# Kernel tuning notes

Hardware: AMD Instinct MI355X
Metric: run time of the kernel (lower is better)

The kernel has to match this reference:

```python
import jax, jax.numpy as jnp
import numpy as np

B, L, D, H = 1, 1024, 768, 12
h = D // H  # 64
EPS = 1e-5
ALPHA = 0.01  # leaky relu slope


def setup_inputs() -> dict:
    key = jax.random.key(0)
    ks = jax.random.split(key, 10)
    s = 0.02
    f32 = jnp.float32
    return {
        "x": jax.random.normal(ks[0], (B, L, D), f32),
        "filters": jax.random.normal(ks[1], (L, h), f32) * s,  # spectral filters [L, h]
        "wq_w": jax.random.normal(ks[2], (D, D), f32) * s,
        "wq_b": jnp.zeros((D,), f32),
        "wk_w": jax.random.normal(ks[3], (D, D), f32) * s,
        "wk_b": jnp.zeros((D,), f32),
        "wv_w": jax.random.normal(ks[4], (D, D), f32) * s,
        "wv_b": jnp.zeros((D,), f32),
        "wo_w": jax.random.normal(ks[5], (D, D), f32) * s,
        "wo_b": jnp.zeros((D,), f32),
        "wg_w": jax.random.normal(ks[6], (h * h, 1), f32) * s,
        "wg_b": jnp.zeros((1,), f32),
        "qk_scale": jnp.ones((1, H, 1), f32) + jax.random.normal(ks[7], (1, H, 1), f32) * 0.02,
        "kv_scale": jnp.ones((1, H, 1, 1, 1), f32) + jax.random.normal(ks[8], (1, H, 1, 1, 1), f32) * 0.02,
    }


def _causal_fft_conv(f, u):
    """Per-head-channel causal FFT convolution. f: [L,h], u: [B,H,L,h] -> [B,H,L,h]."""
    n = 2 * L  # >= L + L - 1 for linear (full) convolution
    Ff = jnp.fft.rfft(f, n=n, axis=0)            # [n//2+1, h]
    Uf = jnp.fft.rfft(u, n=n, axis=2)            # [B,H,n//2+1,h]
    y = jnp.fft.irfft(Uf * Ff[None, None], n=n, axis=2)
    return y[:, :, :L, :]


def _l2norm(t):
    # matches F.normalize(dim=-1): x / max(||x||, 1e-12)
    nrm = jnp.sqrt(jnp.sum(t * t, axis=-1, keepdims=True))
    return t / jnp.maximum(nrm, 1e-12)


def _combine(a, b):
    """Associative combine: (m, s, n, Z, g) running-max / exp-sum / exp-weighted-v / outer-product / gate-sum."""
    m_x, s_x, n_x, Z_x, g_x = a
    m_y, s_y, n_y, Z_y, g_y = b
    m = jnp.maximum(m_x, m_y)
    ex = jnp.exp(m_x - m)
    ey = jnp.exp(m_y - m)
    return (m,
            s_x * ex + s_y * ey,
            n_x * ex[..., None] + n_y * ey[..., None],
            Z_x + Z_y,
            g_x + g_y)


def reference(x, filters, wq_w, wq_b, wk_w, wk_b, wv_w, wv_b, wo_w, wo_b,
              wg_w, wg_b, qk_scale, kv_scale):
    # split heads: [B,H,L,h]
    bhld = x.reshape(B, L, H, h).transpose(0, 2, 1, 3)
    # spectral filtering (tensordot_conv): per-channel causal conv with filters
    xt = _causal_fft_conv(filters, bhld)                       # [B,H,L,h]
    xt = xt.transpose(0, 2, 1, 3).reshape(B, L, D)             # [B,L,D]

    q = (xt @ wq_w + wq_b).reshape(B, L, H, h).transpose(0, 2, 1, 3)
    k = (xt @ wk_w + wk_b).reshape(B, L, H, h).transpose(0, 2, 1, 3)
    v = (xt @ wv_w + wv_b).reshape(B, L, H, h).transpose(0, 2, 1, 3)
    q, k, v = _l2norm(q), _l2norm(k), _l2norm(v)

    sim = jnp.einsum('bhld,bhld->bhl', q, k) * qk_scale         # [B,H,L]
    # Z[b,h,s,p,n] = v[b,h,s,p] * k[b,h,s,n]
    Z = jnp.einsum('bhsn,bhsp->bhspn', k, v) * kv_scale         # [B,H,L,h,h]

    gate_logits = Z.reshape(B, H, L, h * h) @ wg_w + wg_b       # [B,H,L,1]
    gl = jnp.where(gate_logits > 0, gate_logits, ALPHA * gate_logits)
    gates = (gl * gl + EPS)[..., 0]                             # [B,H,L]
    gated_Z = Z * gates[..., None, None]

    leaves = (sim, jnp.ones_like(sim), v, gated_Z, gates)
    m_s, s_s, n_s, Z_s, g_s = jax.lax.associative_scan(_combine, leaves, axis=2)

    linear_attn = n_s / (s_s[..., None] + EPS)                  # [B,H,L,h]
    softmax_w = jnp.exp(sim - m_s) / (s_s + EPS)                # [B,H,L]
    Hm = Z_s / (g_s[..., None, None] + EPS)                     # [B,H,L,h,h]
    ctx = jnp.einsum('bhtp,bhtpn->bhtn', q, Hm)                 # [B,H,L,h]
    qla = linear_attn
    lerp = ctx + (qla - ctx) * softmax_w[..., None]

    y = lerp.transpose(0, 2, 1, 3).reshape(B, L, D)
    return y @ wo_w + wo_b
```

## Files before the change

### kernel.cpp

```cpp
#include <hip/hip_runtime.h>
#include <hip/hip_bf16.h>

constexpr int LS = 1024;
constexpr int DM = 768;
constexpr int NH = 12;
constexpr int HD = 64;
constexpr float EPSF = 1e-5f;
constexpr float ALPHAF = 0.01f;

constexpr int SG = 16;
constexpr int NTL = LS / SG;
constexpr int WSZ = DM * DM;
constexpr int NPAR = 8;

typedef unsigned short u16;
typedef __attribute__((ext_vector_type(8))) short bf16x8;
typedef __attribute__((ext_vector_type(8))) unsigned short u16x8;
typedef __attribute__((ext_vector_type(4))) float f32x4;

__device__ __forceinline__ u16 f2b(float f) {
  unsigned u = __float_as_uint(f);
  u += 0x7FFFu + ((u >> 16) & 1u);
  return (u16)(u >> 16);
}

__device__ __forceinline__ void gld16(const u16* g, void* l) {
  __builtin_amdgcn_global_load_lds(
      (const __attribute__((address_space(1))) void*)g,
      (__attribute__((address_space(3))) void*)l, 16, 0, 0);
}

__global__ __launch_bounds__(256) void conv_txw_kernel(
    const float* __restrict__ x, const float* __restrict__ f,
    const float* __restrict__ wq, const float* __restrict__ wk,
    const float* __restrict__ wv, const float* __restrict__ wo,
    u16* __restrict__ wT, float* __restrict__ pbase) {
  extern __shared__ char smem[];
  const int b = blockIdx.x;
  const int tid = threadIdx.x;

  if (b >= 1536) {
    const int b2 = b - 1536;
    const int kb = (b2 % 12) * 64, nb = ((b2 / 12) % 12) * 64, z = b2 / 144;
    const float* src = (z == 0) ? wq : (z == 1) ? wk : (z == 2) ? wv : wo;
    u16* dst = wT + (size_t)z * WSZ;
    float (*T)[65] = (float(*)[65])smem;
#pragma unroll
    for (int rep = 0; rep < 4; ++rep) {
      const int r = rep * 16 + (tid >> 4);
      const int c4 = (tid & 15) * 4;
      const float4 v4 = *(const float4*)(src + (size_t)(kb + r) * DM + nb + c4);
      T[r][c4] = v4.x; T[r][c4 + 1] = v4.y; T[r][c4 + 2] = v4.z; T[r][c4 + 3] = v4.w;
    }
    __syncthreads();
#pragma unroll
    for (int rep = 0; rep < 4; ++rep) {
      const int n = rep * 16 + (tid >> 4);
      const int k4 = (tid & 15) * 4;
      ushort4 o;
      o.x = f2b(T[k4 + 0][n]); o.y = f2b(T[k4 + 1][n]);
      o.z = f2b(T[k4 + 2][n]); o.w = f2b(T[k4 + 3][n]);
      *(ushort4*)(dst + (size_t)(nb + n) * DM + kb + k4) = o;
    }
    return;
  }

  const int i    = b & 15;
  const int head = (b >> 4) % 12;
  const int par  = b / 192;
  const int c    = tid & 63;
  const int sg   = tid >> 6;
  const int tbase = i * 64;
  const int l0w   = tbase + sg * 16;
  float* __restrict__ xt_p = pbase + (size_t)par * LS * DM;

  float4 (*Xs2)[64] = (float4(*)[64])smem;

  {
    const float4 z4 = make_float4(0.f, 0.f, 0.f, 0.f);
#pragma unroll
    for (int k = 0; k < 3; ++k) {
      const int lin = k * 256 + tid;
      const int g   = lin >> 6;
      const int cc  = lin & 63;
      const int grp = (g < 4) ? g : (16 + g);
      Xs2[grp][cc] = z4;
    }
  }

  float acc[16];
#pragma unroll
  for (int t = 0; t < 16; ++t) acc[t] = 0.f;

  const float* xg   = x + head * HD + c;
  const float* fcol = f + c;

  for (int j = par; j <= i; j += NPAR) {
    const int sbase = j * 64;
    const int b0 = (j < i) ? (tbase - sbase - 64) : 0;
#pragma unroll
    for (int k = 0; k < 4; ++k) {
      const int m  = sg + 4 * k;
      const int ss = 4 * m;
      float4 v4;
      v4.x = xg[(sbase + ss + 0) * DM];
      v4.y = xg[(sbase + ss + 1) * DM];
      v4.z = xg[(sbase + ss + 2) * DM];
      v4.w = xg[(sbase + ss + 3) * DM];
      Xs2[4 + m][c] = v4;
    }
    __syncthreads();

    const int dstart = (j < i) ? (b0 + sg * 16) : 0;
    const int nsteps = (j < i) ? 5 : (sg + 1);
    for (int k = 0; k < nsteps; ++k) {
      const int d0    = dstart + 16 * k;
      const int rbase = l0w - d0 - sbase;
      float fr[16];
#pragma unroll
      for (int m = 0; m < 16; ++m) fr[m] = fcol[(d0 + m) * HD];
      float xw[32];
      const int xgb = rbase >> 2;
#pragma unroll
      for (int m = 0; m < 8; ++m) {
        const float4 v4 = Xs2[xgb + m][c];
        xw[4 * m + 0] = v4.x; xw[4 * m + 1] = v4.y;
        xw[4 * m + 2] = v4.z; xw[4 * m + 3] = v4.w;
      }
#pragma unroll
      for (int li = 0; li < 16; ++li)
#pragma unroll
        for (int dd = 0; dd < 16; ++dd)
          acc[li] = fmaf(fr[dd], xw[li - dd + 16], acc[li]);
    }
    __syncthreads();
  }

#pragma unroll
  for (int li = 0; li < 16; ++li)
    xt_p[(size_t)(l0w + li) * DM + head * HD + c] = acc[li];
}

__global__ __launch_bounds__(256) void pack_xt(const float* __restrict__ pbase,
                                               u16* __restrict__ xtb) {
  const size_t NT = (size_t)LS * DM;
  const size_t i = ((size_t)blockIdx.x * 256 + threadIdx.x) * 8;
  u16x8 o;
#pragma unroll
  for (int h = 0; h < 2; ++h) {
    float4 s = make_float4(0.f, 0.f, 0.f, 0.f);
#pragma unroll
    for (int p = 0; p < NPAR; ++p) {
      const float4 v4 = *(const float4*)(pbase + p * NT + i + h * 4);
      s.x += v4.x; s.y += v4.y; s.z += v4.z; s.w += v4.w;
    }
    o[h * 4 + 0] = f2b(s.x); o[h * 4 + 1] = f2b(s.y);
    o[h * 4 + 2] = f2b(s.z); o[h * 4 + 3] = f2b(s.w);
  }
  *(u16x8*)(xtb + i) = o;
}

__global__ __launch_bounds__(256) void qkv_mfma(const u16* __restrict__ xtb,
                                                const u16* __restrict__ wT,
                                                const float* __restrict__ bq,
                                                const float* __restrict__ bk,
                                                const float* __restrict__ bv,
                                                float* __restrict__ qo,
                                                float* __restrict__ ko,
                                                float* __restrict__ vo) {
  const int b = blockIdx.x;
  const int xcd = b & 7, j = b >> 3;
  const int unit = xcd * 9 + (j >> 3), sub = j & 7;
  const int z = unit / 24, rem = unit % 24;
  const int ct = rem >> 1, rt = (rem & 1) * 8 + sub;

  __shared__ u16 As[64 * 64];
  __shared__ u16 Bs[64 * 64];

  const int tid = threadIdx.x, w = tid >> 6, l = tid & 63;
  const int wr = w >> 1, wc = w & 1;

  const int srow1 = tid >> 3, sc16 = tid & 7;
  const int c16L1 = sc16 ^ (srow1 & 7);
  const int srow2 = srow1 + 32;
  const int c16L2 = sc16 ^ (srow2 & 7);

  const u16* wz = wT + (size_t)z * WSZ;
  const u16* Ag1 = xtb + (size_t)(rt * 64 + srow1) * DM + c16L1 * 8;
  const u16* Ag2 = xtb + (size_t)(rt * 64 + srow2) * DM + c16L2 * 8;
  const u16* Bg1 = wz + (size_t)(ct * 64 + srow1) * DM + c16L1 * 8;
  const u16* Bg2 = wz + (size_t)(ct * 64 + srow2) * DM + c16L2 * 8;

  char* lA = (char*)As + w * 1024;
  char* lB = (char*)Bs + w * 1024;

  f32x4 acc[2][2] = {};
  for (int kb = 0; kb < DM; kb += 64) {
    gld16(Ag1 + kb, lA);
    gld16(Ag2 + kb, lA + 4096);
    gld16(Bg1 + kb, lB);
    gld16(Bg2 + kb, lB + 4096);
    __syncthreads();
#pragma unroll
    for (int kk = 0; kk < 2; ++kk) {
      bf16x8 a[2], bb[2];
#pragma unroll
      for (int ar = 0; ar < 2; ++ar) {
        const int row = wr * 32 + ar * 16 + (l & 15);
        const int c16 = ((kk << 2) + (l >> 4)) ^ (row & 7);
        a[ar] = *(const bf16x8*)((char*)As + row * 128 + c16 * 16);
      }
#pragma unroll
      for (int bc = 0; bc < 2; ++bc) {
        const int col = wc * 32 + bc * 16 + (l & 15);
        const int c16 = ((kk << 2) + (l >> 4)) ^ (col & 7);
        bb[bc] = *(const bf16x8*)((char*)Bs + col * 128 + c16 * 16);
      }
#pragma unroll
      for (int ar = 0; ar < 2; ++ar)
#pragma unroll
        for (int bc = 0; bc < 2; ++bc)
          acc[ar][bc] = __builtin_amdgcn_mfma_f32_16x16x32_bf16(
              a[ar], bb[bc], acc[ar][bc], 0, 0, 0);
    }
    __syncthreads();
  }

  const float* bias = (z == 0) ? bq : (z == 1) ? bk : bv;
  float* out = (z == 0) ? qo : (z == 1) ? ko : vo;
  const int rbase = rt * 64 + wr * 32 + ((l >> 4) << 2);
  const int cb = wc * 32 + (l & 15);
#pragma unroll
  for (int ar = 0; ar < 2; ++ar)
#pragma unroll
    for (int bc = 0; bc < 2; ++bc) {
      const int col = cb + bc * 16;
      const float bbv = bias[ct * 64 + col];
#pragma unroll
      for (int r = 0; r < 4; ++r)
        out[((size_t)ct * LS + rbase + ar * 16 + r) * HD + col] =
            acc[ar][bc][r] + bbv;
    }
}

__global__ __launch_bounds__(256) void out_mfma(const u16* __restrict__ lerpb,
                                                const u16* __restrict__ woT,
                                                const float* __restrict__ bias,
                                                float* __restrict__ out) {
  const int b = blockIdx.x;
  const int xcd = b & 7, j = b >> 3;
  const int unit = xcd * 3 + (j >> 3), sub = j & 7;
  const int ct = unit >> 1, rt = (unit & 1) * 8 + sub;

  __shared__ u16 As[64 * 64];
  __shared__ u16 Bs[64 * 64];

  const int tid = threadIdx.x, w = tid >> 6, l = tid & 63;
  const int wr = w >> 1, wc = w & 1;

  const int srow1 = tid >> 3, sc16 = tid & 7;
  const int c16L1 = sc16 ^ (srow1 & 7);
  const int srow2 = srow1 + 32;
  const int c16L2 = sc16 ^ (srow2 & 7);

  const u16* Ag1 = lerpb + (size_t)(rt * 64 + srow1) * DM + c16L1 * 8;
  const u16* Ag2 = lerpb + (size_t)(rt * 64 + srow2) * DM + c16L2 * 8;
  const u16* Bg1 = woT + (size_t)(ct * 64 + srow1) * DM + c16L1 * 8;
  const u16* Bg2 = woT + (size_t)(ct * 64 + srow2) * DM + c16L2 * 8;

  char* lA = (char*)As + w * 1024;
  char* lB = (char*)Bs + w * 1024;

  f32x4 acc[2][2] = {};
  for (int kb = 0; kb < DM; kb += 64) {
    gld16(Ag1 + kb, lA);
    gld16(Ag2 + kb, lA + 4096);
    gld16(Bg1 + kb, lB);
    gld16(Bg2 + kb, lB + 4096);
    __syncthreads();
#pragma unroll
    for (int kk = 0; kk < 2; ++kk) {
      bf16x8 a[2], bb[2];
#pragma unroll
      for (int ar = 0; ar < 2; ++ar) {
        const int row = wr * 32 + ar * 16 + (l & 15);
        const int c16 = ((kk << 2) + (l >> 4)) ^ (row & 7);
        a[ar] = *(const bf16x8*)((char*)As + row * 128 + c16 * 16);
      }
#pragma unroll
      for (int bc = 0; bc < 2; ++bc) {
        const int col = wc * 32 + bc * 16 + (l & 15);
        const int c16 = ((kk << 2) + (l >> 4)) ^ (col & 7);
        bb[bc] = *(const bf16x8*)((char*)Bs + col * 128 + c16 * 16);
      }
#pragma unroll
      for (int ar = 0; ar < 2; ++ar)
#pragma unroll
        for (int bc = 0; bc < 2; ++bc)
          acc[ar][bc] = __builtin_amdgcn_mfma_f32_16x16x32_bf16(
              a[ar], bb[bc], acc[ar][bc], 0, 0, 0);
    }
    __syncthreads();
  }

  const int rbase = rt * 64 + wr * 32 + ((l >> 4) << 2);
  const int cb = wc * 32 + (l & 15);
#pragma unroll
  for (int ar = 0; ar < 2; ++ar)
#pragma unroll
    for (int bc = 0; bc < 2; ++bc) {
      const int col = ct * 64 + cb + bc * 16;
      const float bbv = bias[col];
#pragma unroll
      for (int r = 0; r < 4; ++r)
        out[(size_t)(rbase + ar * 16 + r) * DM + col] = acc[ar][bc][r] + bbv;
    }
}

__global__ void norm_sim_gate(float* __restrict__ q, float* __restrict__ k, float* __restrict__ v,
                              const float* __restrict__ wg, const float* __restrict__ wgb,
                              const float* __restrict__ qk_scale, const float* __restrict__ kv_scale,
                              float* __restrict__ sim, float* __restrict__ gates) {
  const int w = threadIdx.x >> 6, lane = threadIdx.x & 63;
  const int l = blockIdx.x * 4 + w;
  const int head = blockIdx.y;
  const size_t idx = ((size_t)head * LS + l) * HD + lane;
  float qv = q[idx], kv = k[idx], vv = v[idx];

  auto red = [](float x) {
#pragma unroll
    for (int o = 32; o; o >>= 1) x += __shfl_xor(x, o);
    return x;
  };
  const float qn = fmaxf(sqrtf(red(qv * qv)), 1e-12f);
  const float kn = fmaxf(sqrtf(red(kv * kv)), 1e-12f);
  const float vn = fmaxf(sqrtf(red(vv * vv)), 1e-12f);
  qv /= qn; kv /= kn; vv /= vn;
  q[idx] = qv; k[idx] = kv; v[idx] = vv;

  const float s = red(qv * kv) * qk_scale[head];

  __shared__ float vs[4][64];
  vs[w][lane] = vv;
  __syncthreads();
  float t = 0.f;
#pragma unroll 8
  for (int p = 0; p < 64; ++p) t = fmaf(vs[w][p], wg[p * 64 + lane], t);
  float gl = red(t * kv) * kv_scale[head] + wgb[0];
  gl = gl > 0.f ? gl : ALPHAF * gl;
  const float g = gl * gl + EPSF;
  if (lane == 0) {
    sim[head * LS + l] = s;
    gates[head * LS + l] = g;
  }
}

__global__ void scan_kernel(const float* __restrict__ sim, const float* __restrict__ gates,
                            float* __restrict__ m_s, float* __restrict__ Sraw,
                            float* __restrict__ g_s) {
  const int head = blockIdx.x, t = threadIdx.x;
  __shared__ float bm[1024], bs[1024], bg[1024];
  const float sv = sim[head * LS + t];
  float m = sv, S = expf(sv), g = gates[head * LS + t];
  bm[t] = m; bs[t] = S; bg[t] = g;
  __syncthreads();
  for (int off = 1; off < 1024; off <<= 1) {
    float om = -1e30f, os = 0.f, og = 0.f;
    if (t >= off) { om = bm[t - off]; os = bs[t - off]; og = bg[t - off]; }
    __syncthreads();
    m = fmaxf(m, om); S += os; g += og;
    bm[t] = m; bs[t] = S; bg[t] = g;
    __syncthreads();
  }
  m_s[head * LS + t] = m;
  Sraw[head * LS + t] = S;
  g_s[head * LS + t] = g;
}

__global__ __launch_bounds__(256) void state_kernel(const float* __restrict__ k,
                                                    const float* __restrict__ v,
                                                    const float* __restrict__ sim,
                                                    const float* __restrict__ gates,
                                                    float* __restrict__ states,
                                                    float* __restrict__ nes) {
  const int j = blockIdx.x, head = blockIdx.y;
  const int s0 = j * SG;
  const int tid = threadIdx.x;
  __shared__ alignas(16) float Vs[SG][68];
  __shared__ alignas(16) float Kg[SG][68];
  __shared__ float Es[SG];

  const int r = tid >> 4, c = (tid & 15) * 4;
  const float* kh = k + ((size_t)head * LS + s0) * HD;
  const float* vh = v + ((size_t)head * LS + s0) * HD;
  const float g = gates[head * LS + s0 + r];
  *(float4*)&Vs[r][c] = *(const float4*)(vh + r * HD + c);
  float4 k4 = *(const float4*)(kh + r * HD + c);
  k4.x *= g; k4.y *= g; k4.z *= g; k4.w *= g;
  *(float4*)&Kg[r][c] = k4;
  if (tid < SG) Es[tid] = expf(sim[head * LS + s0 + tid]);
  __syncthreads();

  const int p0 = (tid >> 4) * 4, n0 = (tid & 15) * 4;
  float acc[4][4] = {};
  for (int s = 0; s < SG; ++s) {
    const float4 ra = *(const float4*)&Vs[s][p0];
    const float4 rb = *(const float4*)&Kg[s][n0];
    const float av[4] = {ra.x, ra.y, ra.z, ra.w};
    const float bv[4] = {rb.x, rb.y, rb.z, rb.w};
#pragma unroll
    for (int i = 0; i < 4; ++i)
#pragma unroll
      for (int jj = 0; jj < 4; ++jj)
        acc[i][jj] = fmaf(av[i], bv[jj], acc[i][jj]);
  }
  float* Sout = states + (size_t)(head * NTL + j) * 4096;
#pragma unroll
  for (int i = 0; i < 4; ++i)
    *(float4*)&Sout[(p0 + i) * 64 + n0] =
        make_float4(acc[i][0], acc[i][1], acc[i][2], acc[i][3]);

  if (tid < HD) {
    float ne = 0.f;
    for (int s = 0; s < SG; ++s) ne = fmaf(Es[s], Vs[s][tid], ne);
    nes[(size_t)(head * NTL + j) * HD + tid] = ne;
  }
}

__global__ __launch_bounds__(256) void prefix_kernel(float* __restrict__ states,
                                                     float* __restrict__ nes) {
  const int head = blockIdx.x, chunk = blockIdx.y;
  const int tid = threadIdx.x;
  const int off = chunk * 1024 + tid * 4;
  float4 acc = make_float4(0.f, 0.f, 0.f, 0.f);
  float* base = states + (size_t)head * NTL * 4096 + off;
#pragma unroll 4
  for (int j = 0; j < NTL; ++j) {
    float4* p = (float4*)(base + (size_t)j * 4096);
    const float4 sv = *p;
    *p = acc;
    acc.x += sv.x; acc.y += sv.y; acc.z += sv.z; acc.w += sv.w;
  }
  if (chunk == 0 && tid < HD) {
    float a = 0.f;
    float* nb = nes + (size_t)head * NTL * HD + tid;
#pragma unroll 4
    for (int j = 0; j < NTL; ++j) {
      float* p = nb + (size_t)j * HD;
      const float t = *p;
      *p = a;
      a += t;
    }
  }
}

__global__ __launch_bounds__(256) void apply_kernel(const float* __restrict__ q,
                                                    const float* __restrict__ k,
                                                    const float* __restrict__ v,
                                                    const float* __restrict__ sim,
                                                    const float* __restrict__ gates,
                                                    const float* __restrict__ m_s,
                                                    const float* __restrict__ Sraw,
                                                    const float* __restrict__ g_s,
                                                    const float* __restrict__ states,
                                                    const float* __restrict__ nes,
                                                    const float* __restrict__ kv_scale,
                                                    u16* __restrict__ lerpb) {
  const int bt = blockIdx.x, head = blockIdx.y;
  const int t0 = bt * SG;
  const int tid = threadIdx.x;
  __shared__ alignas(16) float Ps[64][68];
  __shared__ alignas(16) float Qs[SG][68];
  __shared__ alignas(16) float Vs[SG][68];
  __shared__ alignas(16) float Ks[SG][68];
  __shared__ alignas(16) float NEp[64];
  __shared__ float Ag[SG][SG + 1];
  __shared__ float Es[SG], Gs[SG];

  const float* Pg = states + (size_t)(head * NTL + bt) * 4096;
#pragma unroll
  for (int rep = 0; rep < 4; ++rep) {
    const int lin = rep * 1024 + tid * 4;
    *(float4*)&Ps[lin >> 6][lin & 63] = *(const float4*)(Pg + lin);
  }
  {
    const int r = tid >> 4, c = (tid & 15) * 4;
    const size_t rowbase = ((size_t)head * LS + t0 + r) * HD;
    *(float4*)&Qs[r][c] = *(const float4*)(q + rowbase + c);
    *(float4*)&Ks[r][c] = *(const float4*)(k + rowbase + c);
    *(float4*)&Vs[r][c] = *(const float4*)(v + rowbase + c);
  }
  if (tid < SG) {
    Es[tid] = expf(sim[head * LS + t0 + tid]);
    Gs[tid] = gates[head * LS + t0 + tid];
  }
  if (tid < HD) NEp[tid] = nes[(size_t)(head * NTL + bt) * HD + tid];
  __syncthreads();

  {
    const int t = tid >> 4, s = tid & 15;
    float a = 0.f;
    if (s <= t) {
#pragma unroll
      for (int p = 0; p < 64; p += 4) {
        const float4 q4 = *(const float4*)&Qs[t][p];
        const float4 v4 = *(const float4*)&Vs[s][p];
        a = fmaf(q4.x, v4.x, a); a = fmaf(q4.y, v4.y, a);
        a = fmaf(q4.z, v4.z, a); a = fmaf(q4.w, v4.w, a);
      }
      a *= Gs[s];
    }
    Ag[t][s] = a;
  }
  __syncthreads();

  const int r = tid >> 4, c0 = (tid & 15) * 4;
  float4 O = make_float4(0.f, 0.f, 0.f, 0.f);
#pragma unroll 8
  for (int p = 0; p < 64; ++p) {
    const float qv = Qs[r][p];
    const float4 p4 = *(const float4*)&Ps[p][c0];
    O.x = fmaf(qv, p4.x, O.x); O.y = fmaf(qv, p4.y, O.y);
    O.z = fmaf(qv, p4.z, O.z); O.w = fmaf(qv, p4.w, O.w);
  }
  float4 Nn = *(const float4*)&NEp[c0];
  for (int s = 0; s <= r; ++s) {
    const float ag = Ag[r][s];
    const float es = Es[s];
    const float4 k4 = *(const float4*)&Ks[s][c0];
    const float4 v4 = *(const float4*)&Vs[s][c0];
    O.x = fmaf(ag, k4.x, O.x); O.y = fmaf(ag, k4.y, O.y);
    O.z = fmaf(ag, k4.z, O.z); O.w = fmaf(ag, k4.w, O.w);
    Nn.x = fmaf(es, v4.x, Nn.x); Nn.y = fmaf(es, v4.y, Nn.y);
    Nn.z = fmaf(es, v4.z, Nn.z); Nn.w = fmaf(es, v4.w, Nn.w);
  }

  const int t = t0 + r;
  const float m  = m_s[head * LS + t];
  const float em = expf(-m);
  const float ss = Sraw[head * LS + t] * em;
  const float inv = 1.f / (ss + EPSF);
  const float sw  = expf(sim[head * LS + t] - m) * inv;
  const float gi  = kv_scale[head] / (g_s[head * LS + t] + EPSF);
  const float ei  = em * inv;
  float rx, ry, rz, rw;
  { const float cx = O.x * gi, la = Nn.x * ei; rx = cx + (la - cx) * sw; }
  { const float cx = O.y * gi, la = Nn.y * ei; ry = cx + (la - cx) * sw; }
  { const float cx = O.z * gi, la = Nn.z * ei; rz = cx + (la - cx) * sw; }
  { const float cx = O.w * gi, la = Nn.w * ei; rw = cx + (la - cx) * sw; }
  ushort4 ob;
  ob.x = f2b(rx); ob.y = f2b(ry); ob.z = f2b(rz); ob.w = f2b(rw);
  *(ushort4*)&lerpb[(size_t)t * DM + head * HD + c0] = ob;
}

extern "C" void kernel_launch(void* const* d_in, const int* in_sizes, int n_in,
                              void* d_out, int out_size, void* d_ws, size_t ws_size,
                              hipStream_t stream) {
  (void)in_sizes; (void)n_in; (void)out_size; (void)ws_size;
  const float* x        = (const float*)d_in[0];
  const float* filters  = (const float*)d_in[1];
  const float* wq_w     = (const float*)d_in[2];
  const float* wq_b     = (const float*)d_in[3];
  const float* wk_w     = (const float*)d_in[4];
  const float* wk_b     = (const float*)d_in[5];
  const float* wv_w     = (const float*)d_in[6];
  const float* wv_b     = (const float*)d_in[7];
  const float* wo_w     = (const float*)d_in[8];
  const float* wo_b     = (const float*)d_in[9];
  const float* wg_w     = (const float*)d_in[10];
  const float* wg_b     = (const float*)d_in[11];
  const float* qk_scale = (const float*)d_in[12];
  const float* kv_scale = (const float*)d_in[13];

  float* ws = (float*)d_ws;
  const size_t NT = (size_t)LS * DM;
  float* q     = ws;
  float* k     = ws + NT;
  float* v     = ws + 2 * NT;
  float* sim   = ws + 3 * NT;
  float* gates = sim + NH * LS;
  float* m_s   = gates + NH * LS;
  float* Sraw  = m_s + NH * LS;
  float* g_s   = Sraw + NH * LS;
  float* states = g_s + NH * LS;
  float* nes    = states + (size_t)NH * NTL * 4096;
  u16*   xtb    = (u16*)(nes + (size_t)NH * NTL * HD);
  u16*   wT     = xtb + NT;
  u16*   lerpb  = wT + 4 * (size_t)WSZ;
  float* pbase  = (float*)(lerpb + NT);

  conv_txw_kernel<<<dim3(2112), 256, 28672, stream>>>(
      x, filters, wq_w, wk_w, wv_w, wo_w, wT, pbase);
  pack_xt<<<dim3(NT / 2048), 256, 0, stream>>>(pbase, xtb);
  qkv_mfma<<<dim3(576), 256, 0, stream>>>(xtb, wT, wq_b, wk_b, wv_b, q, k, v);
  norm_sim_gate<<<dim3(LS / 4, NH), 256, 0, stream>>>(
      q, k, v, wg_w, wg_b, qk_scale, kv_scale, sim, gates);
  scan_kernel<<<dim3(NH), 1024, 0, stream>>>(sim, gates, m_s, Sraw, g_s);
  state_kernel<<<dim3(NTL, NH), 256, 0, stream>>>(k, v, sim, gates, states, nes);
  prefix_kernel<<<dim3(NH, 4), 256, 0, stream>>>(states, nes);
  apply_kernel<<<dim3(NTL, NH), 256, 0, stream>>>(
      q, k, v, sim, gates, m_s, Sraw, g_s, states, nes, kv_scale, lerpb);
  out_mfma<<<dim3(192), 256, 0, stream>>>(
      lerpb, wT + 3 * (size_t)WSZ, wo_b, (float*)d_out);
}
```

Baseline: 102.5 us.

## Fuse norm/gate into state kernel, fuse scan with prefix, store partials as bf16

Merges the per-row normalize/sim/gate computation into the chunk state kernel, which removes one launch and one global round trip of sim and gates. Merges the scan and prefix kernels into a single 1024-thread kernel whose scan uses warp shuffles with a cross-wave pass instead of a shared-memory Hillis-Steele loop. The conv partial sums are now stored as bf16 instead of fp32, halving pack traffic but adding rounding error before summation. The fused prefix runs on only 12 blocks instead of 48, which reduces parallelism for the state prefix sum.

Result: slower. 107.6 us (+5.0%).

```diff
diff --git a/kernel.cpp b/kernel.cpp
--- a/kernel.cpp
+++ b/kernel.cpp
@@ -23,6 +23,9 @@
   u += 0x7FFFu + ((u >> 16) & 1u);
   return (u16)(u >> 16);
 }
+__device__ __forceinline__ float b2f(u16 b) {
+  return __uint_as_float((unsigned)b << 16);
+}
 
 __device__ __forceinline__ void gld16(const u16* g, void* l) {
   __builtin_amdgcn_global_load_lds(
@@ -34,7 +37,7 @@
     const float* __restrict__ x, const float* __restrict__ f,
     const float* __restrict__ wq, const float* __restrict__ wk,
     const float* __restrict__ wv, const float* __restrict__ wo,
-    u16* __restrict__ wT, float* __restrict__ pbase) {
+    u16* __restrict__ wT, u16* __restrict__ pbase) {
   extern __shared__ char smem[];
   const int b = blockIdx.x;
   const int tid = threadIdx.x;
@@ -72,7 +75,7 @@
   const int sg   = tid >> 6;
   const int tbase = i * 64;
   const int l0w   = tbase + sg * 16;
-  float* __restrict__ xt_p = pbase + (size_t)par * LS * DM;
+  u16* __restrict__ xt_p = pbase + (size_t)par * LS * DM;
 
   float4 (*Xs2)[64] = (float4(*)[64])smem;
 
@@ -138,25 +141,23 @@
 
 #pragma unroll
   for (int li = 0; li < 16; ++li)
-    xt_p[(size_t)(l0w + li) * DM + head * HD + c] = acc[li];
-}
-
-__global__ __launch_bounds__(256) void pack_xt(const float* __restrict__ pbase,
+    xt_p[(size_t)(l0w + li) * DM + head * HD + c] = f2b(acc[li]);
+}
+
+__global__ __launch_bounds__(256) void pack_xt(const u16* __restrict__ pbase,
                                                u16* __restrict__ xtb) {
   const size_t NT = (size_t)LS * DM;
   const size_t i = ((size_t)blockIdx.x * 256 + threadIdx.x) * 8;
+  float s[8] = {};
+#pragma unroll
+  for (int p = 0; p < NPAR; ++p) {
+    const u16x8 v8 = *(const u16x8*)(pbase + p * NT + i);
+#pragma unroll
+    for (int e = 0; e < 8; ++e) s[e] += b2f(v8[e]);
+  }
   u16x8 o;
 #pragma unroll
-  for (int h = 0; h < 2; ++h) {
-    float4 s = make_float4(0.f, 0.f, 0.f, 0.f);
-#pragma unroll
-    for (int p = 0; p < NPAR; ++p) {
-      const float4 v4 = *(const float4*)(pbase + p * NT + i + h * 4);
-      s.x += v4.x; s.y += v4.y; s.z += v4.z; s.w += v4.w;
-    }
-    o[h * 4 + 0] = f2b(s.x); o[h * 4 + 1] = f2b(s.y);
-    o[h * 4 + 2] = f2b(s.z); o[h * 4 + 3] = f2b(s.w);
-  }
+  for (int e = 0; e < 8; ++e) o[e] = f2b(s[e]);
   *(u16x8*)(xtb + i) = o;
 }
 
@@ -317,88 +318,52 @@
     }
 }
 
-__global__ void norm_sim_gate(float* __restrict__ q, float* __restrict__ k, float* __restrict__ v,
-                              const float* __restrict__ wg, const float* __restrict__ wgb,
-                              const float* __restrict__ qk_scale, const float* __restrict__ kv_scale,
-                              float* __restrict__ sim, float* __restrict__ gates) {
-  const int w = threadIdx.x >> 6, lane = threadIdx.x & 63;
-  const int l = blockIdx.x * 4 + w;
-  const int head = blockIdx.y;
-  const size_t idx = ((size_t)head * LS + l) * HD + lane;
-  float qv = q[idx], kv = k[idx], vv = v[idx];
+__global__ __launch_bounds__(256) void nsg_state_kernel(
+    float* __restrict__ q, float* __restrict__ k, float* __restrict__ v,
+    const float* __restrict__ wg, const float* __restrict__ wgb,
+    const float* __restrict__ qk_scale, const float* __restrict__ kv_scale,
+    float* __restrict__ sim, float* __restrict__ gates,
+    float* __restrict__ states, float* __restrict__ nes) {
+  const int j = blockIdx.x, head = blockIdx.y;
+  const int s0 = j * SG;
+  const int tid = threadIdx.x;
+  const int wid = tid >> 6, lane = tid & 63;
+  __shared__ alignas(16) float Vs[SG][68];
+  __shared__ alignas(16) float Kg[SG][68];
+  __shared__ float Es[SG];
 
   auto red = [](float x) {
 #pragma unroll
     for (int o = 32; o; o >>= 1) x += __shfl_xor(x, o);
     return x;
   };
-  const float qn = fmaxf(sqrtf(red(qv * qv)), 1e-12f);
-  const float kn = fmaxf(sqrtf(red(kv * kv)), 1e-12f);
-  const float vn = fmaxf(sqrtf(red(vv * vv)), 1e-12f);
-  qv /= qn; kv /= kn; vv /= vn;
-  q[idx] = qv; k[idx] = kv; v[idx] = vv;
-
-  const float s = red(qv * kv) * qk_scale[head];
-
-  __shared__ float vs[4][64];
-  vs[w][lane] = vv;
-  __syncthreads();
-  float t = 0.f;
+
+  const float qks = qk_scale[head], kvs = kv_scale[head], wb = wgb[0];
+#pragma unroll
+  for (int it = 0; it < 4; ++it) {
+    const int rr = wid * 4 + it;
+    const size_t idx = ((size_t)head * LS + s0 + rr) * HD + lane;
+    float qv = q[idx], kv = k[idx], vv = v[idx];
+    const float qn = fmaxf(sqrtf(red(qv * qv)), 1e-12f);
+    const float kn = fmaxf(sqrtf(red(kv * kv)), 1e-12f);
+    const float vn = fmaxf(sqrtf(red(vv * vv)), 1e-12f);
+    qv /= qn; kv /= kn; vv /= vn;
+    q[idx] = qv; k[idx] = kv; v[idx] = vv;
+    const float s = red(qv * kv) * qks;
+    Vs[rr][lane] = vv;
+    float t = 0.f;
 #pragma unroll 8
-  for (int p = 0; p < 64; ++p) t = fmaf(vs[w][p], wg[p * 64 + lane], t);
-  float gl = red(t * kv) * kv_scale[head] + wgb[0];
-  gl = gl > 0.f ? gl : ALPHAF * gl;
-  const float g = gl * gl + EPSF;
-  if (lane == 0) {
-    sim[head * LS + l] = s;
-    gates[head * LS + l] = g;
-  }
-}
-
-__global__ void scan_kernel(const float* __restrict__ sim, const float* __restrict__ gates,
-                            float* __restrict__ m_s, float* __restrict__ Sraw,
-                            float* __restrict__ g_s) {
-  const int head = blockIdx.x, t = threadIdx.x;
-  __shared__ float bm[1024], bs[1024], bg[1024];
-  const float sv = sim[head * LS + t];
-  float m = sv, S = expf(sv), g = gates[head * LS + t];
-  bm[t] = m; bs[t] = S; bg[t] = g;
-  __syncthreads();
-  for (int off = 1; off < 1024; off <<= 1) {
-    float om = -1e30f, os = 0.f, og = 0.f;
-    if (t >= off) { om = bm[t - off]; os = bs[t - off]; og = bg[t - off]; }
-    __syncthreads();
-    m = fmaxf(m, om); S += os; g += og;
-    bm[t] = m; bs[t] = S; bg[t] = g;
-    __syncthreads();
-  }
-  m_s[head * LS + t] = m;
-  Sraw[head * LS + t] = S;
-  g_s[head * LS + t] = g;
-}
-
-__global__ __launch_bounds__(256) void state_kernel(const float* __restrict__ k,
-                                                    const float* __restrict__ v,
-                                                    const float* __restrict__ sim,
-                                                    const float* __restrict__ gates,
-                                                    float* __restrict__ states,
-                                                    float* __restrict__ nes) {
-  const int j = blockIdx.x, head = blockIdx.y;
-  const int s0 = j * SG;
-  const int tid = threadIdx.x;
-  __shared__ alignas(16) float Vs[SG][68];
-  __shared__ alignas(16) float Kg[SG][68];
-  __shared__ float Es[SG];
-
-  const int r = tid >> 4, c = (tid & 15) * 4;
-  const float* kh = k + ((size_t)head * LS + s0) * HD;
-  const float* vh = v + ((size_t)head * LS + s0) * HD;
-  const float g = gates[head * LS + s0 + r];
-  *(float4*)&Vs[r][c] = *(const float4*)(vh + r * HD + c);
-  float4 k4 = *(const float4*)(kh + r * HD + c);
-  k4.x *= g; k4.y *= g; k4.z *= g; k4.w *= g;
-  *(float4*)&Kg[r][c] = k4;
-  if (tid < SG) Es[tid] = expf(sim[head * LS + s0 + tid]);
+    for (int p = 0; p < 64; ++p) t = fmaf(Vs[rr][p], wg[p * 64 + lane], t);
+    float gl = red(t * kv) * kvs + wb;
+    gl = gl > 0.f ? gl : ALPHAF * gl;
+    const float g = gl * gl + EPSF;
+    Kg[rr][lane] = kv * g;
+    if (lane == 0) {
+      sim[head * LS + s0 + rr] = s;
+      gates[head * LS + s0 + rr] = g;
+      Es[rr] = expf(s);
+    }
+  }
   __syncthreads();
 
   const int p0 = (tid >> 4) * 4, n0 = (tid & 15) * 4;
@@ -422,31 +387,55 @@
 
   if (tid < HD) {
     float ne = 0.f;
+#pragma unroll
     for (int s = 0; s < SG; ++s) ne = fmaf(Es[s], Vs[s][tid], ne);
     nes[(size_t)(head * NTL + j) * HD + tid] = ne;
   }
 }
 
-__global__ __launch_bounds__(256) void prefix_kernel(float* __restrict__ states,
-                                                     float* __restrict__ nes) {
-  const int head = blockIdx.x, chunk = blockIdx.y;
-  const int tid = threadIdx.x;
-  const int off = chunk * 1024 + tid * 4;
-  float4 acc = make_float4(0.f, 0.f, 0.f, 0.f);
-  float* base = states + (size_t)head * NTL * 4096 + off;
+__global__ __launch_bounds__(1024) void scan_prefix_kernel(
+    const float* __restrict__ sim, const float* __restrict__ gates,
+    float* __restrict__ m_s, float* __restrict__ Sraw, float* __restrict__ g_s,
+    float* __restrict__ states, float* __restrict__ nes) {
+  const int head = blockIdx.x;
+  const int tid = threadIdx.x, lane = tid & 63, wid = tid >> 6;
+  __shared__ float wm[16], wS[16], wg2[16];
+
+  const float sv = sim[head * LS + tid];
+  float m = sv, S = expf(sv), g = gates[head * LS + tid];
+#pragma unroll
+  for (int off = 1; off < 64; off <<= 1) {
+    const float pm = __shfl_up(m, off);
+    const float pS = __shfl_up(S, off);
+    const float pg = __shfl_up(g, off);
+    if (lane >= off) { m = fmaxf(m, pm); S += pS; g += pg; }
+  }
+  if (lane == 63) { wm[wid] = m; wS[wid] = S; wg2[wid] = g; }
+  __syncthreads();
+  for (int w2 = 0; w2 < wid; ++w2) {
+    m = fmaxf(m, wm[w2]); S += wS[w2]; g += wg2[w2];
+  }
+  m_s[head * LS + tid] = m;
+  Sraw[head * LS + tid] = S;
+  g_s[head * LS + tid] = g;
+
+  {
+    float4 acc = make_float4(0.f, 0.f, 0.f, 0.f);
+    float* base = states + (size_t)head * NTL * 4096 + tid * 4;
 #pragma unroll 4
-  for (int j = 0; j < NTL; ++j) {
-    float4* p = (float4*)(base + (size_t)j * 4096);
-    const float4 sv = *p;
-    *p = acc;
-    acc.x += sv.x; acc.y += sv.y; acc.z += sv.z; acc.w += sv.w;
-  }
-  if (chunk == 0 && tid < HD) {
+    for (int jj = 0; jj < NTL; ++jj) {
+      float4* p = (float4*)(base + (size_t)jj * 4096);
+      const float4 s4 = *p;
+      *p = acc;
+      acc.x += s4.x; acc.y += s4.y; acc.z += s4.z; acc.w += s4.w;
+    }
+  }
+  if (tid < HD) {
     float a = 0.f;
     float* nb = nes + (size_t)head * NTL * HD + tid;
 #pragma unroll 4
-    for (int j = 0; j < NTL; ++j) {
-      float* p = nb + (size_t)j * HD;
+    for (int jj = 0; jj < NTL; ++jj) {
+      float* p = nb + (size_t)jj * HD;
       const float t = *p;
       *p = a;
       a += t;
@@ -587,17 +576,16 @@
   u16*   xtb    = (u16*)(nes + (size_t)NH * NTL * HD);
   u16*   wT     = xtb + NT;
   u16*   lerpb  = wT + 4 * (size_t)WSZ;
-  float* pbase  = (float*)(lerpb + NT);
+  u16*   pbase  = lerpb + NT;
 
   conv_txw_kernel<<<dim3(2112), 256, 28672, stream>>>(
       x, filters, wq_w, wk_w, wv_w, wo_w, wT, pbase);
   pack_xt<<<dim3(NT / 2048), 256, 0, stream>>>(pbase, xtb);
   qkv_mfma<<<dim3(576), 256, 0, stream>>>(xtb, wT, wq_b, wk_b, wv_b, q, k, v);
-  norm_sim_gate<<<dim3(LS / 4, NH), 256, 0, stream>>>(
-      q, k, v, wg_w, wg_b, qk_scale, kv_scale, sim, gates);
-  scan_kernel<<<dim3(NH), 1024, 0, stream>>>(sim, gates, m_s, Sraw, g_s);
-  state_kernel<<<dim3(NTL, NH), 256, 0, stream>>>(k, v, sim, gates, states, nes);
-  prefix_kernel<<<dim3(NH, 4), 256, 0, stream>>>(states, nes);
+  nsg_state_kernel<<<dim3(NTL, NH), 256, 0, stream>>>(
+      q, k, v, wg_w, wg_b, qk_scale, kv_scale, sim, gates, states, nes);
+  scan_prefix_kernel<<<dim3(NH), 1024, 0, stream>>>(
+      sim, gates, m_s, Sraw, g_s, states, nes);
   apply_kernel<<<dim3(NTL, NH), 256, 0, stream>>>(
       q, k, v, sim, gates, m_s, Sraw, g_s, states, nes, kv_scale, lerpb);
   out_mfma<<<dim3(192), 256, 0, stream>>>(
```
